# Kernel tuning notes

Measured on AMD Instinct MI355X. Metric: run time of the kernel, lower is better.

Reference implementation:

```python
import jax, jax.numpy as jnp
import numpy as np

B, S, D, H = 2, 2048, 1024, 16
DK = D // H


def setup_inputs() -> dict:
    key = jax.random.key(0)
    ks = jax.random.split(key, 12)
    s = 0.02
    return {
        "q": jax.random.normal(ks[0], (B, S, D), jnp.float32),
        "k": jax.random.normal(ks[1], (B, S, D), jnp.float32),
        "v": jax.random.normal(ks[2], (B, S, D), jnp.float32),
        "mask": jax.random.randint(ks[3], (1, 1, S, S), 0, 2, jnp.int32),
        "Wq": jax.random.normal(ks[4], (D, D), jnp.float32) * s,
        "bq": jnp.zeros((D,), jnp.float32),
        "Wk": jax.random.normal(ks[5], (D, D), jnp.float32) * s,
        "bk": jnp.zeros((D,), jnp.float32),
        "Wv": jax.random.normal(ks[6], (D, D), jnp.float32) * s,
        "bv": jnp.zeros((D,), jnp.float32),
        "Wo": jax.random.normal(ks[7], (D, D), jnp.float32) * s,
        "bo": jnp.zeros((D,), jnp.float32),
    }


def reference(q, k, v, mask, Wq, bq, Wk, bk, Wv, bv, Wo, bo):
    # linear projections (torch Linear: x @ W.T + b)
    qp = q @ Wq.T + bq
    kp = k @ Wk.T + bk
    vp = v @ Wv.T + bv
    # [B, S, D] -> [B, H, S, DK]
    split = lambda x: x.reshape(B, S, H, DK).transpose(0, 2, 1, 3)
    qh, kh, vh = split(qp), split(kp), split(vp)
    scale = 1.0 / jnp.sqrt(jnp.float32(DK))
    attn = jnp.einsum('bhsd,bhtd->bhst', qh, kh) * scale  # [B,H,S,S]
    attn = jnp.where(mask == 0, jnp.float32(-1e9), attn)
    attn = jax.nn.softmax(attn, axis=-1)
    out = jnp.einsum('bhst,bhtd->bhsd', attn, vh)  # [B,H,S,DK]
    concat = out.transpose(0, 2, 1, 3).reshape(B, S, D)
    return concat @ Wo.T + bo
```

## Files before the change

### kernel.cpp

```cpp
#include <hip/hip_runtime.h>
#include <hip/hip_bf16.h>


using bf16x8 = __attribute__((ext_vector_type(8))) short;
using f32x4  = __attribute__((ext_vector_type(4))) float;
using f32x16 = __attribute__((ext_vector_type(16))) float;

constexpr int Bc = 2, Sc = 2048, Dc = 1024, Hc = 16, DKc = 64;
constexpr int Mc = Bc * Sc;
#define QSCALE 0.18033688011112042f

__device__ __forceinline__ void lds_load16(const void* g, void* l) {
  __builtin_amdgcn_global_load_lds(
      (const __attribute__((address_space(1))) unsigned int*)g,
      (__attribute__((address_space(3))) unsigned int*)l, 16, 0, 0);
}

#if __has_builtin(__builtin_amdgcn_exp2f)
__device__ __forceinline__ float exp2_fast(float x) { return __builtin_amdgcn_exp2f(x); }
#else
__device__ __forceinline__ float exp2_fast(float x) {
  float r;
  asm("v_exp_f32 %0, %1\n\ts_nop 0" : "=v"(r) : "v"(x));
  return r;
}
#endif

__device__ __forceinline__ unsigned cvt_pk_bf16(float lo, float hi) {
  unsigned r;
  asm("v_cvt_pk_bf16_f32 %0, %1, %2" : "=v"(r) : "v"(lo), "v"(hi));
  return r;
}

#define PSWAP(A, B) \
  asm volatile("v_permlane32_swap_b32 %0, %1" : "+v"(A), "+v"(B))

__device__ __forceinline__ unsigned pack2bf(float a, float b) {
  union { __hip_bfloat16 h; unsigned short s; } ua, ub;
  ua.h = __float2bfloat16(a);
  ub.h = __float2bfloat16(b);
  return (unsigned)ua.s | ((unsigned)ub.s << 16);
}

__global__ void prep(const float* __restrict__ q, const float* __restrict__ k,
                     const float* __restrict__ v, const int* __restrict__ mask,
                     const float* __restrict__ Wq, const float* __restrict__ Wk,
                     const float* __restrict__ Wv, const float* __restrict__ Wo,
                     char* __restrict__ ws) {
  const size_t MB = 1024 * 1024;
  int blk = blockIdx.x;
  if (blk < 12288) {
    int which = blk >> 12;
    int i = (((blk & 4095) << 8) + threadIdx.x) * 4;
    const float* s = which == 0 ? q : (which == 1 ? k : v);
    __hip_bfloat16* d = (__hip_bfloat16*)(ws + (size_t)which * 8 * MB);
    float4 x = *(const float4*)&s[i];
    uint2 pk = {pack2bf(x.x, x.y), pack2bf(x.z, x.w)};
    *(uint2*)&d[i] = pk;
  } else if (blk < 16384) {
    int bb = blk - 12288;
    int which = bb >> 10;
    int i = (((bb & 1023) << 8) + threadIdx.x) * 4;
    const float* s = which == 0 ? Wq : (which == 1 ? Wk : (which == 2 ? Wv : Wo));
    __hip_bfloat16* d = which < 3 ? (__hip_bfloat16*)(ws + (24 + 2 * which) * MB)
                                  : (__hip_bfloat16*)(ws + 30 * MB);
    float4 x = *(const float4*)&s[i];
    uint2 pk = {pack2bf(x.x, x.y), pack2bf(x.z, x.w)};
    *(uint2*)&d[i] = pk;
  } else {
    int i = ((blk - 16384) << 8) + threadIdx.x;
    unsigned long long bal = __ballot(mask[i] != 0);
    if ((threadIdx.x & 63) == 0)
      ((unsigned long long*)(ws + 32 * MB))[i >> 6] = bal;
  }
}

__global__ __launch_bounds__(256, 3) void proj_qkv(
    const __hip_bfloat16* __restrict__ qb, const __hip_bfloat16* __restrict__ kb,
    const __hip_bfloat16* __restrict__ vb, const __hip_bfloat16* __restrict__ Wcat,
    const float* __restrict__ bq, const float* __restrict__ bk,
    const float* __restrict__ bv, __hip_bfloat16* __restrict__ qhd,
    __hip_bfloat16* __restrict__ khd, __hip_bfloat16* __restrict__ vtd) {
  __shared__ __align__(16) __hip_bfloat16 As[2][128 * 32];
  __shared__ __align__(16) __hip_bfloat16 Bs[2][128 * 32];
  const int tid = threadIdx.x;
  const int f = blockIdx.x, g = f >> 3;
  const int m0 = ((f & 7) * 4 + g / 24) * 128;
  const int n0 = (g % 24) * 128;
  const int which = n0 >> 10, nl0 = n0 & 1023;
  const __hip_bfloat16* X = which == 0 ? qb : (which == 1 ? kb : vb);
  const float* bias = which == 0 ? bq : (which == 1 ? bk : bv);
  const int w = tid >> 6, lane = tid & 63, ln = lane & 15, quad = lane >> 4;
  const int rl = w * 32 + (lane >> 2);
  const int sw8 = ((lane & 3) ^ ((lane >> 2) & 3)) * 8;
  const int aoff = (n0 + rl) * 1024 + sw8;
  const int boff = (m0 + rl) * 1024 + sw8;
  char* aDst = (char*)As + w * 2048 + lane * 16;
  char* bDst = (char*)Bs + w * 2048 + lane * 16;
  const int rkq = (quad ^ (ln & 3)) * 16;
  const int rA0 = ((w >> 1) * 64 + ln) * 64 + rkq;
  const int rB0 = ((w & 1) * 64 + ln) * 64 + rkq;
  f32x4 acc[4][4] = {};

#define PSTAGE(KO, BI)                                                        \
  {                                                                           \
    lds_load16(&Wcat[aoff + (KO)], aDst + (BI)*8192);                         \
    lds_load16(&Wcat[aoff + 16384 + (KO)], aDst + (BI)*8192 + 1024);          \
    lds_load16(&X[boff + (KO)], bDst + (BI)*8192);                            \
    lds_load16(&X[boff + 16384 + (KO)], bDst + (BI)*8192 + 1024);             \
  }

  PSTAGE(0, 0);
  if (which == 2) {
    for (int kb32 = 0; kb32 < 32; ++kb32) {
      const int bi = kb32 & 1;
      __syncthreads();
      if (kb32 < 31) PSTAGE((kb32 + 1) * 32, bi ^ 1);
      bf16x8 af[4], bf[4];
#pragma unroll
      for (int i = 0; i < 4; ++i)
        af[i] = *(bf16x8*)((char*)As + bi * 8192 + rA0 + i * 1024);
#pragma unroll
      for (int j = 0; j < 4; ++j)
        bf[j] = *(bf16x8*)((char*)Bs + bi * 8192 + rB0 + j * 1024);
#pragma unroll
      for (int i = 0; i < 4; ++i)
#pragma unroll
        for (int j = 0; j < 4; ++j)
          acc[i][j] = __builtin_amdgcn_mfma_f32_16x16x32_bf16(bf[j], af[i],
                                                              acc[i][j], 0, 0, 0);
    }
  } else {
    for (int kb32 = 0; kb32 < 32; ++kb32) {
      const int bi = kb32 & 1;
      __syncthreads();
      if (kb32 < 31) PSTAGE((kb32 + 1) * 32, bi ^ 1);
      bf16x8 af[4], bf[4];
#pragma unroll
      for (int i = 0; i < 4; ++i)
        af[i] = *(bf16x8*)((char*)As + bi * 8192 + rA0 + i * 1024);
#pragma unroll
      for (int j = 0; j < 4; ++j)
        bf[j] = *(bf16x8*)((char*)Bs + bi * 8192 + rB0 + j * 1024);
#pragma unroll
      for (int i = 0; i < 4; ++i)
#pragma unroll
        for (int j = 0; j < 4; ++j)
          acc[i][j] = __builtin_amdgcn_mfma_f32_16x16x32_bf16(af[i], bf[j],
                                                              acc[i][j], 0, 0, 0);
    }
  }

  const int wA = (w >> 1) * 64, wB = (w & 1) * 64;
  if (which == 2) {
#pragma unroll
    for (int i = 0; i < 4; ++i) {
      int nf = nl0 + wA + i * 16 + ln;
      int h = nf >> 6, dk = nf & 63;
      float bb = bias[nf];
#pragma unroll
      for (int j = 0; j < 4; ++j) {
        int sb = m0 + wB + j * 16 + quad * 4;
        int b = sb >> 11, s = sb & 2047;
        float vv[4] = {acc[i][j][0] + bb, acc[i][j][1] + bb,
                       acc[i][j][2] + bb, acc[i][j][3] + bb};
        uint2 pk = {pack2bf(vv[0], vv[1]), pack2bf(vv[2], vv[3])};
        *(uint2*)&vtd[(((size_t)(b * Hc + h) * DKc + dk) * Sc) + s] = pk;
      }
    }
  } else {
#pragma unroll
    for (int i = 0; i < 4; ++i) {
      int nfb = nl0 + wA + i * 16 + quad * 4;
      float4 b4 = *(const float4*)&bias[nfb];
      int h = nfb >> 6, dk0 = nfb & 63;
#pragma unroll
      for (int j = 0; j < 4; ++j) {
        int sg = m0 + wB + j * 16 + ln;
        int b = sg >> 11, s = sg & 2047;
        float vv[4] = {acc[i][j][0] + b4.x, acc[i][j][1] + b4.y,
                       acc[i][j][2] + b4.z, acc[i][j][3] + b4.w};
        if (which == 0) {
          uint2 pk = {pack2bf(vv[0] * QSCALE, vv[1] * QSCALE),
                      pack2bf(vv[2] * QSCALE, vv[3] * QSCALE)};
          *(uint2*)&qhd[(((size_t)(b * Hc + h) * Sc + s) * DKc) + dk0] = pk;
        } else {
          uint2 pk = {pack2bf(vv[0], vv[1]), pack2bf(vv[2], vv[3])};
          *(uint2*)&khd[(((size_t)(b * Hc + h) * Sc + s) * DKc) + dk0] = pk;
        }
      }
    }
  }
}

__global__ __launch_bounds__(256, 2) void gemm_out(
    const __hip_bfloat16* __restrict__ X, const __hip_bfloat16* __restrict__ W,
    const float* __restrict__ bias, float* __restrict__ Y) {
  __shared__ __align__(16) __hip_bfloat16 As[2][64 * 64];
  __shared__ __align__(16) __hip_bfloat16 Bs[2][128 * 64];
  const int tid = threadIdx.x;
  const int f = blockIdx.x, g = f >> 3;
  const int m0 = ((f & 7) * 4 + (g >> 4)) * 128;
  const int n0 = (g & 15) * 64;
  const int w = tid >> 6, lane = tid & 63, ln = lane & 15, quad = lane >> 4;
  const int wA = (w & 1) * 32, wB = (w >> 1) * 64;
  const int swz = ((lane & 7) ^ (lane >> 3)) * 8;
  const int rk0 = ln * 128 + ((quad ^ (ln & 7)) * 16);
  const int rk1 = ln * 128 + (((quad + 4) ^ (ln & 7)) * 16);
  const int aoff = (n0 + w * 16 + (lane >> 3)) * 1024 + swz;
  const int boff = (m0 + w * 32 + (lane >> 3)) * 1024 + swz;
  f32x4 acc[2][4] = {};

#define OSTAGE(KO, BI)                                                        \
  {                                                                           \
    _Pragma("unroll") for (int i = 0; i < 2; ++i)                             \
        lds_load16(&W[aoff + i * 8192 + (KO)],                                \
                   (char*)As[BI] + w * 2048 + lane * 16 + i * 1024);          \
    _Pragma("unroll") for (int i = 0; i < 4; ++i)                             \
        lds_load16(&X[boff + i * 8192 + (KO)],                                \
                   (char*)Bs[BI] + w * 4096 + lane * 16 + i * 1024);          \
  }

  OSTAGE(0, 0);
  for (int kb64 = 0; kb64 < 16; ++kb64) {
    const int bi = kb64 & 1;
    __syncthreads();
    if (kb64 + 1 < 16) OSTAGE((kb64 + 1) * 64, bi ^ 1);
    bf16x8 af[2][2], bf[4][2];
#pragma unroll
    for (int i = 0; i < 2; ++i) {
      af[i][0] = *(bf16x8*)((char*)As[bi] + wA * 128 + i * 2048 + rk0);
      af[i][1] = *(bf16x8*)((char*)As[bi] + wA * 128 + i * 2048 + rk1);
    }
#pragma unroll
    for (int j = 0; j < 4; ++j) {
      bf[j][0] = *(bf16x8*)((char*)Bs[bi] + wB * 128 + j * 2048 + rk0);
      bf[j][1] = *(bf16x8*)((char*)Bs[bi] + wB * 128 + j * 2048 + rk1);
    }
#pragma unroll
    for (int i = 0; i < 2; ++i)
#pragma unroll
      for (int j = 0; j < 4; ++j) {
        acc[i][j] = __builtin_amdgcn_mfma_f32_16x16x32_bf16(af[i][0], bf[j][0],
                                                            acc[i][j], 0, 0, 0);
        acc[i][j] = __builtin_amdgcn_mfma_f32_16x16x32_bf16(af[i][1], bf[j][1],
                                                            acc[i][j], 0, 0, 0);
      }
  }
#pragma unroll
  for (int i = 0; i < 2; ++i) {
    int nfb = n0 + wA + i * 16 + quad * 4;
    float4 b4 = *(const float4*)&bias[nfb];
#pragma unroll
    for (int j = 0; j < 4; ++j) {
      int sg = m0 + wB + j * 16 + ln;
      float4 st = {acc[i][j][0] + b4.x, acc[i][j][1] + b4.y,
                   acc[i][j][2] + b4.z, acc[i][j][3] + b4.w};
      *(float4*)&Y[(size_t)sg * Dc + nfb] = st;
    }
  }
}

__global__ __launch_bounds__(256, 2) void flash_attn(
    const __hip_bfloat16* __restrict__ qh, const __hip_bfloat16* __restrict__ kh,
    const __hip_bfloat16* __restrict__ vt, const uint2* __restrict__ mb2,
    __hip_bfloat16* __restrict__ oc) {
  __shared__ __align__(16) char L[32768];
  const int tid = threadIdx.x;
  const int f = blockIdx.x, g = f >> 3;
  const int bh = (f & 7) * 4 + (g >> 4);
  const int q0 = (g & 15) * 128;
  const int b = bh >> 4, h = bh & 15;
  const int w = tid >> 6, lane = tid & 63, l31 = lane & 31, hi = lane >> 5;
  const size_t base = (size_t)bh * Sc * DKc;
  const __hip_bfloat16* khb = kh + base;
  const __hip_bfloat16* vtb = vt + base;
  const int qglob = q0 + w * 32 + l31;

  bf16x8 qf[4];
#pragma unroll
  for (int dt = 0; dt < 4; ++dt)
    qf[dt] = *(const bf16x8*)&qh[base + (size_t)qglob * 64 + dt * 16 + hi * 8];

  bf16x8 onesA;
#pragma unroll
  for (int i = 0; i < 8; ++i) onesA[i] = (short)0x3F80;

  const int trow = tid >> 3, tcol = tid & 7;
  const int kbase = trow * 64 + ((tcol ^ (trow & 7)) * 8);
  const int vbase = trow * 2048 + ((tcol ^ (trow & 7)) * 8);
  char* Ld = L + tid * 16;

  const int rowb = l31 * 128;
  const int xs = lane & 7;

  f32x16 Oacc0 = {}, Oacc1 = {}, lacc = {};

#define STAGE(BI, T)                                                          \
  {                                                                           \
    lds_load16(khb + kbase + (T)*4096,        Ld + (BI)*8192);                \
    lds_load16(khb + kbase + (T)*4096 + 2048, Ld + (BI)*8192 + 4096);         \
    lds_load16(vtb + vbase + (T)*64,          Ld + 16384 + (BI)*8192);        \
    lds_load16(vtb + vbase + (T)*64 + 65536,  Ld + 16384 + (BI)*8192 + 4096); \
  }

#define PROC_SUB(BOFF, SUB, MW)                                               \
  {                                                                           \
    bf16x8 kf0 = *(bf16x8*)(L + (BOFF) + (SUB)*4096 + rowb + (((0 + hi) ^ xs) * 16)); \
    bf16x8 kf1 = *(bf16x8*)(L + (BOFF) + (SUB)*4096 + rowb + (((2 + hi) ^ xs) * 16)); \
    bf16x8 kf2 = *(bf16x8*)(L + (BOFF) + (SUB)*4096 + rowb + (((4 + hi) ^ xs) * 16)); \
    bf16x8 kf3 = *(bf16x8*)(L + (BOFF) + (SUB)*4096 + rowb + (((6 + hi) ^ xs) * 16)); \
    f32x16 c = {};                                                            \
    __builtin_amdgcn_s_setprio(1);                                            \
    c = __builtin_amdgcn_mfma_f32_32x32x16_bf16(kf0, qf[0], c, 0, 0, 0);      \
    c = __builtin_amdgcn_mfma_f32_32x32x16_bf16(kf1, qf[1], c, 0, 0, 0);      \
    c = __builtin_amdgcn_mfma_f32_32x32x16_bf16(kf2, qf[2], c, 0, 0, 0);      \
    c = __builtin_amdgcn_mfma_f32_32x32x16_bf16(kf3, qf[3], c, 0, 0, 0);      \
    __builtin_amdgcn_s_setprio(0);                                            \
    unsigned shm = (MW) >> (hi * 4);                                          \
    float p[16];                                                              \
    _Pragma("unroll") for (int r = 0; r < 16; ++r) {                          \
      unsigned tg = shm >> (8 * (r >> 2));                                    \
      float e = exp2_fast(c[r]);                                              \
      p[r] = (tg & (1u << (r & 3))) ? e : 0.f;                                \
    }                                                                         \
    unsigned w0 = cvt_pk_bf16(p[0], p[1]),   w1 = cvt_pk_bf16(p[2], p[3]);    \
    unsigned w2 = cvt_pk_bf16(p[4], p[5]),   w3 = cvt_pk_bf16(p[6], p[7]);    \
    unsigned w4 = cvt_pk_bf16(p[8], p[9]),   w5 = cvt_pk_bf16(p[10], p[11]);  \
    unsigned w6 = cvt_pk_bf16(p[12], p[13]), w7 = cvt_pk_bf16(p[14], p[15]);  \
    PSWAP(w0, w2); PSWAP(w1, w3); PSWAP(w4, w6); PSWAP(w5, w7);               \
    { union { unsigned u[4]; bf16x8 v; } t;                                   \
      t.u[0] = w0; t.u[1] = w1; t.u[2] = w2; t.u[3] = w3;                     \
      pb[(SUB)*2] = t.v; }                                                    \
    { union { unsigned u[4]; bf16x8 v; } t;                                   \
      t.u[0] = w4; t.u[1] = w5; t.u[2] = w6; t.u[3] = w7;                     \
      pb[(SUB)*2 + 1] = t.v; }                                                \
  }

  const uint2* mrow = mb2 + (size_t)qglob * 32;
  uint2 mbC = mrow[0];
  STAGE(0, 0);

  for (int t = 0; t < 32; ++t) {
    __syncthreads();
    uint2 mbN = mbC;
    if (t < 31) {
      mbN = mrow[t + 1];
      STAGE((t + 1) & 1, t + 1);
    }
    const int boff = (t & 1) * 8192;

    bf16x8 pb[4];
    PROC_SUB(boff, 0, mbC.x);
    PROC_SUB(boff, 1, mbC.y);

    __builtin_amdgcn_s_setprio(1);
#pragma unroll
    for (int kt = 0; kt < 4; ++kt) {
      lacc = __builtin_amdgcn_mfma_f32_32x32x16_bf16(onesA, pb[kt], lacc, 0, 0, 0);
      bf16x8 vf0 = *(bf16x8*)(L + 16384 + boff + rowb + (((kt * 2 + hi) ^ xs) * 16));
      bf16x8 vf1 = *(bf16x8*)(L + 16384 + boff + 4096 + rowb + (((kt * 2 + hi) ^ xs) * 16));
      Oacc0 = __builtin_amdgcn_mfma_f32_32x32x16_bf16(vf0, pb[kt], Oacc0, 0, 0, 0);
      Oacc1 = __builtin_amdgcn_mfma_f32_32x32x16_bf16(vf1, pb[kt], Oacc1, 0, 0, 0);
    }
    __builtin_amdgcn_s_setprio(0);
    mbC = mbN;
  }

  float linv = 1.f / fmaxf(lacc[0], 1e-30f);
  const size_t obase = (size_t)(b * Sc + qglob) * Dc + h * 64;
#pragma unroll
  for (int gq = 0; gq < 4; ++gq) {
    int d0 = gq * 8 + hi * 4;
    uint2 pk0 = {pack2bf(Oacc0[4 * gq] * linv, Oacc0[4 * gq + 1] * linv),
                 pack2bf(Oacc0[4 * gq + 2] * linv, Oacc0[4 * gq + 3] * linv)};
    *(uint2*)&oc[obase + d0] = pk0;
    uint2 pk1 = {pack2bf(Oacc1[4 * gq] * linv, Oacc1[4 * gq + 1] * linv),
                 pack2bf(Oacc1[4 * gq + 2] * linv, Oacc1[4 * gq + 3] * linv)};
    *(uint2*)&oc[obase + 32 + d0] = pk1;
  }
#undef STAGE
#undef PROC_SUB
}

extern "C" void kernel_launch(void* const* d_in, const int* in_sizes, int n_in,
                              void* d_out, int out_size, void* d_ws, size_t ws_size,
                              hipStream_t stream) {
  const float* q  = (const float*)d_in[0];
  const float* k  = (const float*)d_in[1];
  const float* v  = (const float*)d_in[2];
  const int* mask = (const int*)d_in[3];
  const float* Wq = (const float*)d_in[4];
  const float* bq = (const float*)d_in[5];
  const float* Wk = (const float*)d_in[6];
  const float* bk = (const float*)d_in[7];
  const float* Wv = (const float*)d_in[8];
  const float* bv = (const float*)d_in[9];
  const float* Wo = (const float*)d_in[10];
  const float* bo = (const float*)d_in[11];

  char* ws = (char*)d_ws;
  const size_t MB = 1024 * 1024;
  __hip_bfloat16* qb   = (__hip_bfloat16*)(ws + 0 * MB);
  __hip_bfloat16* kb   = (__hip_bfloat16*)(ws + 8 * MB);
  __hip_bfloat16* vb   = (__hip_bfloat16*)(ws + 16 * MB);
  __hip_bfloat16* Wcat = (__hip_bfloat16*)(ws + 24 * MB);
  __hip_bfloat16* Wob  = (__hip_bfloat16*)(ws + 30 * MB);
  uint2*          mb2  = (uint2*)(ws + 32 * MB);
  __hip_bfloat16* qhd  = (__hip_bfloat16*)(ws + 33 * MB);
  __hip_bfloat16* khd  = (__hip_bfloat16*)(ws + 41 * MB);
  __hip_bfloat16* vtd  = (__hip_bfloat16*)(ws + 49 * MB);
  __hip_bfloat16* oc   = (__hip_bfloat16*)(ws + 57 * MB);

  prep<<<32768, 256, 0, stream>>>(q, k, v, mask, Wq, Wk, Wv, Wo, ws);
  proj_qkv<<<768, 256, 0, stream>>>(qb, kb, vb, Wcat, bq, bk, bv, qhd, khd, vtd);
  flash_attn<<<512, 256, 0, stream>>>(qhd, khd, vtd, mb2, oc);
  gemm_out<<<512, 256, 0, stream>>>(oc, Wob, bo, (float*)d_out);
}
```

Before: 243.8 us.

## Fuse fp32-to-bf16 activation conversion into QKV projection loads

Removes the separate prep pass that converted q/k/v activations to bf16. The projection kernel now loads fp32 activations into registers, converts them, and writes them to LDS after the MFMA block, so the global loads overlap compute. The prep kernel also vectorises the weight conversion and packs the mask bits with 16-byte loads and shuffles. This cuts a full round trip of activation traffic, at the cost of more registers and VGPR-staged LDS writes in place of direct global-to-LDS loads. Each projection block also re-reads activations from fp32, which doubles the bytes per re-read.

```diff
diff --git a/kernel.cpp b/kernel.cpp
--- a/kernel.cpp
+++ b/kernel.cpp
@@ -42,42 +42,42 @@
   return (unsigned)ua.s | ((unsigned)ub.s << 16);
 }
 
-__global__ void prep(const float* __restrict__ q, const float* __restrict__ k,
-                     const float* __restrict__ v, const int* __restrict__ mask,
+__global__ void prep(const int* __restrict__ mask,
                      const float* __restrict__ Wq, const float* __restrict__ Wk,
                      const float* __restrict__ Wv, const float* __restrict__ Wo,
                      char* __restrict__ ws) {
   const size_t MB = 1024 * 1024;
   int blk = blockIdx.x;
-  if (blk < 12288) {
-    int which = blk >> 12;
-    int i = (((blk & 4095) << 8) + threadIdx.x) * 4;
-    const float* s = which == 0 ? q : (which == 1 ? k : v);
-    __hip_bfloat16* d = (__hip_bfloat16*)(ws + (size_t)which * 8 * MB);
+  int tid = threadIdx.x;
+  if (blk < 2048) {
+    int which = blk >> 9;
+    int i = (((blk & 511) << 8) + tid) * 8;
+    const float* s = which == 0 ? Wq : (which == 1 ? Wk : (which == 2 ? Wv : Wo));
+    __hip_bfloat16* d = (__hip_bfloat16*)(ws + (size_t)2 * which * MB);
     float4 x = *(const float4*)&s[i];
-    uint2 pk = {pack2bf(x.x, x.y), pack2bf(x.z, x.w)};
-    *(uint2*)&d[i] = pk;
-  } else if (blk < 16384) {
-    int bb = blk - 12288;
-    int which = bb >> 10;
-    int i = (((bb & 1023) << 8) + threadIdx.x) * 4;
-    const float* s = which == 0 ? Wq : (which == 1 ? Wk : (which == 2 ? Wv : Wo));
-    __hip_bfloat16* d = which < 3 ? (__hip_bfloat16*)(ws + (24 + 2 * which) * MB)
-                                  : (__hip_bfloat16*)(ws + 30 * MB);
-    float4 x = *(const float4*)&s[i];
-    uint2 pk = {pack2bf(x.x, x.y), pack2bf(x.z, x.w)};
-    *(uint2*)&d[i] = pk;
+    float4 y = *(const float4*)&s[i + 4];
+    uint4 pk = {pack2bf(x.x, x.y), pack2bf(x.z, x.w),
+                pack2bf(y.x, y.y), pack2bf(y.z, y.w)};
+    *(uint4*)&d[i] = pk;
   } else {
-    int i = ((blk - 16384) << 8) + threadIdx.x;
-    unsigned long long bal = __ballot(mask[i] != 0);
-    if ((threadIdx.x & 63) == 0)
-      ((unsigned long long*)(ws + 32 * MB))[i >> 6] = bal;
+    int blkm = blk - 2048;
+    int i0 = ((blkm << 8) + tid) * 4;
+    uint4 m = *(const uint4*)&mask[i0];
+    unsigned nib = (m.x != 0 ? 1u : 0u) | (m.y != 0 ? 2u : 0u) |
+                   (m.z != 0 ? 4u : 0u) | (m.w != 0 ? 8u : 0u);
+    unsigned long long w = (unsigned long long)nib << (4 * (tid & 15));
+    w |= __shfl_xor(w, 1);
+    w |= __shfl_xor(w, 2);
+    w |= __shfl_xor(w, 4);
+    w |= __shfl_xor(w, 8);
+    if ((tid & 15) == 0)
+      ((unsigned long long*)(ws + 8 * MB))[(blkm << 4) + (tid >> 4)] = w;
   }
 }
 
 __global__ __launch_bounds__(256, 3) void proj_qkv(
-    const __hip_bfloat16* __restrict__ qb, const __hip_bfloat16* __restrict__ kb,
-    const __hip_bfloat16* __restrict__ vb, const __hip_bfloat16* __restrict__ Wcat,
+    const float* __restrict__ qf_, const float* __restrict__ kf_,
+    const float* __restrict__ vf_, const __hip_bfloat16* __restrict__ Wcat,
     const float* __restrict__ bq, const float* __restrict__ bk,
     const float* __restrict__ bv, __hip_bfloat16* __restrict__ qhd,
     __hip_bfloat16* __restrict__ khd, __hip_bfloat16* __restrict__ vtd) {
@@ -88,7 +88,7 @@
   const int m0 = ((f & 7) * 4 + g / 24) * 128;
   const int n0 = (g % 24) * 128;
   const int which = n0 >> 10, nl0 = n0 & 1023;
-  const __hip_bfloat16* X = which == 0 ? qb : (which == 1 ? kb : vb);
+  const float* X = which == 0 ? qf_ : (which == 1 ? kf_ : vf_);
   const float* bias = which == 0 ? bq : (which == 1 ? bk : bv);
   const int w = tid >> 6, lane = tid & 63, ln = lane & 15, quad = lane >> 4;
   const int rl = w * 32 + (lane >> 2);
@@ -102,20 +102,38 @@
   const int rB0 = ((w & 1) * 64 + ln) * 64 + rkq;
   f32x4 acc[4][4] = {};
 
-#define PSTAGE(KO, BI)                                                        \
+#define PSTAGE_A(KO, BI)                                                      \
   {                                                                           \
     lds_load16(&Wcat[aoff + (KO)], aDst + (BI)*8192);                         \
     lds_load16(&Wcat[aoff + 16384 + (KO)], aDst + (BI)*8192 + 1024);          \
-    lds_load16(&X[boff + (KO)], bDst + (BI)*8192);                            \
-    lds_load16(&X[boff + 16384 + (KO)], bDst + (BI)*8192 + 1024);             \
-  }
-
-  PSTAGE(0, 0);
+  }
+#define PLOADX(KO)                                                            \
+  {                                                                           \
+    x0 = *(const float4*)&X[boff + (KO)];                                     \
+    x1 = *(const float4*)&X[boff + (KO) + 4];                                 \
+    x2 = *(const float4*)&X[boff + 16384 + (KO)];                             \
+    x3 = *(const float4*)&X[boff + 16384 + (KO) + 4];                         \
+  }
+#define PWRITEX(BI)                                                           \
+  {                                                                           \
+    union { unsigned u[4]; bf16x8 v; } t0, t1;                                \
+    t0.u[0] = pack2bf(x0.x, x0.y); t0.u[1] = pack2bf(x0.z, x0.w);             \
+    t0.u[2] = pack2bf(x1.x, x1.y); t0.u[3] = pack2bf(x1.z, x1.w);             \
+    t1.u[0] = pack2bf(x2.x, x2.y); t1.u[1] = pack2bf(x2.z, x2.w);             \
+    t1.u[2] = pack2bf(x3.x, x3.y); t1.u[3] = pack2bf(x3.z, x3.w);             \
+    *(bf16x8*)(bDst + (BI)*8192) = t0.v;                                      \
+    *(bf16x8*)(bDst + (BI)*8192 + 1024) = t1.v;                               \
+  }
+
+  float4 x0, x1, x2, x3;
+  PSTAGE_A(0, 0);
+  PLOADX(0);
+  PWRITEX(0);
   if (which == 2) {
     for (int kb32 = 0; kb32 < 32; ++kb32) {
       const int bi = kb32 & 1;
       __syncthreads();
-      if (kb32 < 31) PSTAGE((kb32 + 1) * 32, bi ^ 1);
+      if (kb32 < 31) { PSTAGE_A((kb32 + 1) * 32, bi ^ 1); PLOADX((kb32 + 1) * 32); }
       bf16x8 af[4], bf[4];
 #pragma unroll
       for (int i = 0; i < 4; ++i)
@@ -129,12 +147,13 @@
         for (int j = 0; j < 4; ++j)
           acc[i][j] = __builtin_amdgcn_mfma_f32_16x16x32_bf16(bf[j], af[i],
                                                               acc[i][j], 0, 0, 0);
+      if (kb32 < 31) PWRITEX(bi ^ 1);
     }
   } else {
     for (int kb32 = 0; kb32 < 32; ++kb32) {
       const int bi = kb32 & 1;
       __syncthreads();
-      if (kb32 < 31) PSTAGE((kb32 + 1) * 32, bi ^ 1);
+      if (kb32 < 31) { PSTAGE_A((kb32 + 1) * 32, bi ^ 1); PLOADX((kb32 + 1) * 32); }
       bf16x8 af[4], bf[4];
 #pragma unroll
       for (int i = 0; i < 4; ++i)
@@ -148,6 +167,7 @@
         for (int j = 0; j < 4; ++j)
           acc[i][j] = __builtin_amdgcn_mfma_f32_16x16x32_bf16(af[i], bf[j],
                                                               acc[i][j], 0, 0, 0);
+      if (kb32 < 31) PWRITEX(bi ^ 1);
     }
   }
 
@@ -401,19 +421,16 @@
 
   char* ws = (char*)d_ws;
   const size_t MB = 1024 * 1024;
-  __hip_bfloat16* qb   = (__hip_bfloat16*)(ws + 0 * MB);
-  __hip_bfloat16* kb   = (__hip_bfloat16*)(ws + 8 * MB);
-  __hip_bfloat16* vb   = (__hip_bfloat16*)(ws + 16 * MB);
-  __hip_bfloat16* Wcat = (__hip_bfloat16*)(ws + 24 * MB);
-  __hip_bfloat16* Wob  = (__hip_bfloat16*)(ws + 30 * MB);
-  uint2*          mb2  = (uint2*)(ws + 32 * MB);
-  __hip_bfloat16* qhd  = (__hip_bfloat16*)(ws + 33 * MB);
-  __hip_bfloat16* khd  = (__hip_bfloat16*)(ws + 41 * MB);
-  __hip_bfloat16* vtd  = (__hip_bfloat16*)(ws + 49 * MB);
-  __hip_bfloat16* oc   = (__hip_bfloat16*)(ws + 57 * MB);
-
-  prep<<<32768, 256, 0, stream>>>(q, k, v, mask, Wq, Wk, Wv, Wo, ws);
-  proj_qkv<<<768, 256, 0, stream>>>(qb, kb, vb, Wcat, bq, bk, bv, qhd, khd, vtd);
+  __hip_bfloat16* Wcat = (__hip_bfloat16*)(ws + 0 * MB);
+  __hip_bfloat16* Wob  = (__hip_bfloat16*)(ws + 6 * MB);
+  uint2*          mb2  = (uint2*)(ws + 8 * MB);
+  __hip_bfloat16* qhd  = (__hip_bfloat16*)(ws + 9 * MB);
+  __hip_bfloat16* khd  = (__hip_bfloat16*)(ws + 17 * MB);
+  __hip_bfloat16* vtd  = (__hip_bfloat16*)(ws + 25 * MB);
+  __hip_bfloat16* oc   = (__hip_bfloat16*)(ws + 33 * MB);
+
+  prep<<<6144, 256, 0, stream>>>(mask, Wq, Wk, Wv, Wo, ws);
+  proj_qkv<<<768, 256, 0, stream>>>(q, k, v, Wcat, bq, bk, bv, qhd, khd, vtd);
   flash_attn<<<512, 256, 0, stream>>>(qhd, khd, vtd, mb2, oc);
   gemm_out<<<512, 256, 0, stream>>>(oc, Wob, bo, (float*)d_out);
 }
```

Measured after the change: 247.3 us. Within noise of the previous version (+1.4%).
